# Optimization experiments

Hardware: AMD Instinct MI355X
Metric: run time of the kernel (lower is better)

The kernel has to match this reference:

```python
import jax, jax.numpy as jnp
import numpy as np

N_NODES = 100000
N_EDGES = 1600000
D_FEAT = 128
HIDDEN = 64


def setup_inputs() -> dict:
    key = jax.random.key(0)
    k1, k2, k3, k4, k5 = jax.random.split(key, 5)
    x = jax.random.normal(k1, (N_NODES, D_FEAT), dtype=jnp.float32)
    edge_index = jax.random.randint(k2, (2, N_EDGES), 0, N_NODES, dtype=jnp.int32)
    edge_weight = jax.random.uniform(k3, (N_EDGES,), dtype=jnp.float32)
    W1 = jax.random.normal(k4, (D_FEAT, HIDDEN), dtype=jnp.float32) / np.sqrt(D_FEAT)
    b1 = jnp.zeros((HIDDEN,), dtype=jnp.float32)
    W2 = jax.random.normal(k5, (HIDDEN, 1), dtype=jnp.float32) / np.sqrt(HIDDEN)
    b2 = jnp.zeros((1,), dtype=jnp.float32)
    return {"x": x, "edge_index": edge_index, "edge_weight": edge_weight,
            "W1": W1, "b1": b1, "W2": W2, "b2": b2}


def reference(x, edge_index, edge_weight, W1, b1, W2, b2):
    N = x.shape[0]
    # PyG GCNConv default: add self-loops with weight 1.0
    loops = jnp.arange(N, dtype=edge_index.dtype)
    row = jnp.concatenate([edge_index[0], loops])  # source nodes
    col = jnp.concatenate([edge_index[1], loops])  # target nodes
    ew = jnp.concatenate([edge_weight, jnp.ones((N,), dtype=edge_weight.dtype)])
    # symmetric degree normalization: norm_e = d^{-1/2}[row] * w_e * d^{-1/2}[col]
    deg = jax.ops.segment_sum(ew, col, num_segments=N)
    dinv = jnp.where(deg > 0, jax.lax.rsqrt(deg), 0.0)
    norm = dinv[row] * ew * dinv[col]  # [E+N]

    def gcn_layer(h, W, b):
        h = h @ W                          # [N, out] transform first (PyG order)
        msg = h[row] * norm[:, None]       # gather + scale, [E+N, out]
        agg = jax.ops.segment_sum(msg, col, num_segments=N)  # scatter-add
        return agg + b

    h = jax.nn.relu(gcn_layer(x, W1, b1))
    # dropout(p=0.5) is identity in eval mode
    return gcn_layer(h, W2, b2)  # [N, 1]
```

## Files before the change

kernel.cpp:

```cpp
#include <hip/hip_runtime.h>
#include <stdint.h>

typedef float f4 __attribute__((ext_vector_type(4)));
typedef float f32x4 __attribute__((ext_vector_type(4)));
typedef _Float16 hq4 __attribute__((ext_vector_type(4)));
typedef _Float16 half8 __attribute__((ext_vector_type(8)));

#define DF 128
#define HID 64
#define EPB 4096
#define CAP 5120

__global__ __launch_bounds__(256) void kPrep(const float* __restrict__ W1,
                                             _Float16* __restrict__ W1f,
                                             int* __restrict__ cur, int nbin) {
    int t = blockIdx.x * 256 + threadIdx.x;
    if (t < nbin) cur[t] = 0;
    if (t < 8192) {
        int j     = t & 7;
        int lane  = (t >> 3) & 63;
        int ntile = (t >> 9) & 3;
        int kstep = t >> 11;
        int k = kstep * 32 + (lane >> 4) * 8 + j;
        int n = ntile * 16 + (lane & 15);
        W1f[t] = (_Float16)W1[k * 64 + n];
    }
}

__global__ __launch_bounds__(512) void kA3(const int* __restrict__ row,
                                           const int* __restrict__ col,
                                           const float* __restrict__ ew,
                                           int* __restrict__ cur,
                                           int2* __restrict__ tmp,
                                           int E, int nbin) {
    __shared__ int hist[512];
    __shared__ int pref[512];
    __shared__ int lbase[512];
    __shared__ int2 sv[EPB];
    __shared__ int  sa[EPB];
    int b = blockIdx.x, t = threadIdx.x;
    hist[t] = 0;
    __syncthreads();
    int s = b * EPB, e = min(E, s + EPB);
    int cnt = e - s;
    int  mybin[8], myrank[8];
    int2 myv[8];
#pragma unroll
    for (int k = 0; k < 8; ++k) {
        int i = s + t + k * 512;
        mybin[k] = -1;
        if (i < e) {
            int c = col[i];
            int bin = c >> 8;
            myv[k].x = row[i] | ((c & 255) << 24);
            myv[k].y = __float_as_int(ew[i]);
            mybin[k] = bin;
            myrank[k] = atomicAdd(&hist[bin], 1);
        }
    }
    __syncthreads();
    int val = hist[t];
    lbase[t] = val ? atomicAdd(&cur[t], val) + t * CAP : 0;
    for (int d = 1; d < 512; d <<= 1) {
        int x = (t >= d) ? hist[t - d] : 0;
        __syncthreads();
        hist[t] += x;
        __syncthreads();
    }
    pref[t] = hist[t] - val;
    __syncthreads();
#pragma unroll
    for (int k = 0; k < 8; ++k) {
        if (mybin[k] >= 0) {
            int pos = pref[mybin[k]] + myrank[k];
            sv[pos] = myv[k];
            sa[pos] = lbase[mybin[k]] + myrank[k];
        }
    }
    __syncthreads();
    for (int i = t; i < cnt; i += 512) tmp[sa[i]] = sv[i];
}

__global__ __launch_bounds__(256) void kB(const int2* __restrict__ tmp,
                                          const int* __restrict__ cur,
                                          int2* __restrict__ edata,
                                          int2* __restrict__ offse,
                                          float* __restrict__ dinv,
                                          int N) {
    __shared__ int hist[256];
    __shared__ int basel[256];
    __shared__ int startl[256];
    __shared__ float degl[256];
    __shared__ int2 sorted[CAP];
    int bin = blockIdx.x, t = threadIdx.x;
    int s = bin * CAP;
    int cnt = min(cur[bin], CAP);
    int e = s + cnt;

    hist[t] = 0;
    degl[t] = 0.f;
    __syncthreads();
    for (int i = s + t; i < e; i += 256) {
        int2 pr = tmp[i];
        int lo = ((unsigned)pr.x) >> 24;
        atomicAdd(&hist[lo], 1);
        atomicAdd(&degl[lo], __int_as_float(pr.y));
    }
    __syncthreads();
    int val = hist[t];
    __syncthreads();
    for (int d = 1; d < 256; d <<= 1) {
        int x = (t >= d) ? hist[t - d] : 0;
        __syncthreads();
        hist[t] += x;
        __syncthreads();
    }
    int loff = hist[t] - val;
    startl[t] = s + loff;
    basel[t]  = loff;
    __syncthreads();
    for (int i = s + t; i < e; i += 256) {
        int2 pr = tmp[i];
        int lo = ((unsigned)pr.x) >> 24;
        int pos = atomicAdd(&basel[lo], 1);
        int2 o;
        o.x = pr.x & 0x00FFFFFF;
        o.y = pr.y;
        sorted[pos] = o;
    }
    __syncthreads();
    for (int i = t; i < cnt; i += 256) edata[s + i] = sorted[i];
    int c = bin * 256 + t;
    if (c < N) {
        int2 oe;
        oe.x = startl[t];
        oe.y = startl[t] + val;
        offse[c] = oe;
        dinv[c] = rsqrtf(1.0f + degl[t]);
    }
}

__global__ __launch_bounds__(256) void k_gemm1(const float* __restrict__ x,
                                               const _Float16* __restrict__ W1f,
                                               const float* __restrict__ dinv,
                                               _Float16* __restrict__ h, int N) {
    int wave  = (blockIdx.x * 256 + threadIdx.x) >> 6;
    int nstrip = (N + 15) >> 4;
    if (wave >= nstrip) return;
    int node0 = wave << 4;
    int l = threadIdx.x & 63;
    int quad = l >> 4;
    int m = l & 15;
    int r = node0 + m;
    if (r >= N) r = N - 1;

    const half8* bfrag = (const half8*)W1f;
    f32x4 acc[4];
#pragma unroll
    for (int nt = 0; nt < 4; ++nt) acc[nt] = (f32x4)(0.f);

#pragma unroll
    for (int kstep = 0; kstep < 4; ++kstep) {
        const f4* xr = (const f4*)(x + (size_t)r * DF + kstep * 32 + quad * 8);
        f4 a0 = xr[0], a1 = xr[1];
        half8 af;
        af[0] = (_Float16)a0.x; af[1] = (_Float16)a0.y;
        af[2] = (_Float16)a0.z; af[3] = (_Float16)a0.w;
        af[4] = (_Float16)a1.x; af[5] = (_Float16)a1.y;
        af[6] = (_Float16)a1.z; af[7] = (_Float16)a1.w;
#pragma unroll
        for (int nt = 0; nt < 4; ++nt) {
            half8 bf = bfrag[(kstep * 4 + nt) * 64 + l];
            acc[nt] = __builtin_amdgcn_mfma_f32_16x16x32_f16(af, bf, acc[nt], 0, 0, 0);
        }
    }

    float dv[4];
    int nodeb = node0 + quad * 4;
#pragma unroll
    for (int reg = 0; reg < 4; ++reg)
        dv[reg] = (nodeb + reg < N) ? dinv[nodeb + reg] : 0.f;
#pragma unroll
    for (int nt = 0; nt < 4; ++nt) {
#pragma unroll
        for (int reg = 0; reg < 4; ++reg) {
            int node = nodeb + reg;
            if (node < N)
                h[(unsigned)node * 64u + (unsigned)(nt * 16 + m)] =
                    (_Float16)(dv[reg] * acc[nt][reg]);
        }
    }
}

__global__ __launch_bounds__(256) void k_agg_h2(const int2* __restrict__ offse,
                                                const int2* __restrict__ edata,
                                                const float* __restrict__ dinv,
                                                const _Float16* __restrict__ h,
                                                const float* __restrict__ b1,
                                                const float* __restrict__ W2,
                                                float* __restrict__ h2p, int N) {
    __shared__ int2 stage[4][64];
    int wv = threadIdx.x >> 6;
    int v = blockIdx.x * 4 + wv;
    if (v >= N) return;
    int l = threadIdx.x & 63;
    int sub = l >> 4;
    unsigned fq = (unsigned)(l & 15);
    const hq4* hp = (const hq4*)h;

    float di = dinv[v];
    float a0 = 0.f, a1 = 0.f, a2 = 0.f, a3 = 0.f;
    if (sub == 0) {
        hq4 sv4 = hp[((unsigned)v << 4) | fq];
        a0 = (float)sv4.x; a1 = (float)sv4.y;
        a2 = (float)sv4.z; a3 = (float)sv4.w;
    }

    int2 oe = offse[v];
    for (int base = oe.x; base < oe.y; base += 64) {
        int idx = base + l;
        int2 pr;
        pr.x = 0; pr.y = 0;
        if (idx < oe.y) pr = edata[idx];
        stage[wv][l] = pr;
        int cnt = min(64, oe.y - base);
        int steps = (cnt + 3) >> 2;
#pragma unroll 4
        for (int k = 0; k < steps; ++k) {
            int2 em = stage[wv][4 * k + sub];
            float w = __int_as_float(em.y);
            hq4 hv = hp[((unsigned)em.x << 4) | fq];
            a0 += w * (float)hv.x;
            a1 += w * (float)hv.y;
            a2 += w * (float)hv.z;
            a3 += w * (float)hv.w;
        }
    }
    a0 += __shfl_xor(a0, 16); a1 += __shfl_xor(a1, 16);
    a2 += __shfl_xor(a2, 16); a3 += __shfl_xor(a3, 16);
    a0 += __shfl_xor(a0, 32); a1 += __shfl_xor(a1, 32);
    a2 += __shfl_xor(a2, 32); a3 += __shfl_xor(a3, 32);

    if (sub == 0) {
        a0 = di * a0; a1 = di * a1; a2 = di * a2; a3 = di * a3;
        float s = fmaxf(a0 + b1[4 * fq], 0.f)     * W2[4 * fq]
                + fmaxf(a1 + b1[4 * fq + 1], 0.f) * W2[4 * fq + 1]
                + fmaxf(a2 + b1[4 * fq + 2], 0.f) * W2[4 * fq + 2]
                + fmaxf(a3 + b1[4 * fq + 3], 0.f) * W2[4 * fq + 3];
        s += __shfl_down(s, 8);
        s += __shfl_down(s, 4);
        s += __shfl_down(s, 2);
        s += __shfl_down(s, 1);
        if (fq == 0) h2p[v] = di * s;
    }
}

__global__ __launch_bounds__(256) void k_out(const int2* __restrict__ offse,
                                             const int2* __restrict__ edata,
                                             const float* __restrict__ dinv,
                                             const float* __restrict__ h2p,
                                             const float* __restrict__ b2,
                                             float* __restrict__ out, int N) {
    int t = blockIdx.x * 256 + threadIdx.x;
    int v = t >> 4;
    if (v >= N) return;
    int c = t & 15;
    int2 oe = offse[v];
    float s = 0.f;
    for (int i = oe.x + c; i < oe.y; i += 16) {
        int2 pr = edata[i];
        s += __int_as_float(pr.y) * h2p[(unsigned)pr.x];
    }
    s += __shfl_down(s, 8);
    s += __shfl_down(s, 4);
    s += __shfl_down(s, 2);
    s += __shfl_down(s, 1);
    if (c == 0) {
        float di = dinv[v];
        out[v] = b2[0] + di * (h2p[v] + s);
    }
}

extern "C" void kernel_launch(void* const* d_in, const int* in_sizes, int n_in,
                              void* d_out, int out_size, void* d_ws, size_t ws_size,
                              hipStream_t stream) {
    const float* x  = (const float*)d_in[0];
    const int*   ei = (const int*)d_in[1];
    const float* ew = (const float*)d_in[2];
    const float* W1 = (const float*)d_in[3];
    const float* b1 = (const float*)d_in[4];
    const float* W2 = (const float*)d_in[5];
    const float* b2 = (const float*)d_in[6];
    float* out = (float*)d_out;

    const int N = in_sizes[0] / DF;
    const int E = in_sizes[2];
    const int* row = ei;
    const int* col = ei + E;

    const int nbin = (N + 255) / 256;
    const int nblk = (E + EPB - 1) / EPB;

    size_t    gsz   = (size_t)nbin * CAP;
    int*      w32   = (int*)d_ws;
    int2*     edata = (int2*)w32;
    int*      shreg = w32 + (size_t)2 * gsz;
    int2*     tmp   = (int2*)shreg;
    _Float16* h     = (_Float16*)shreg;
    int*      p     = shreg + (size_t)2 * gsz;
    int*      cur   = p;  p += ((nbin) + 3) & ~3;
    float*    dinv  = (float*)p;  p += N;
    float*    h2p   = (float*)p;  p += N;
    int2*     offse = (int2*)p;   p += 2 * N;
    _Float16* W1f   = (_Float16*)p;

    const int B = 256;
    int nstrip = (N + 15) / 16;
    int gGm  = (nstrip + 3) / 4;
    int gAgg = (N + 3) / 4;
    int gN16 = (N * 16 + B - 1) / B;

    kPrep<<<32, B, 0, stream>>>(W1, W1f, cur, nbin);
    kA3<<<nblk, 512, 0, stream>>>(row, col, ew, cur, tmp, E, nbin);
    kB<<<nbin, B, 0, stream>>>(tmp, cur, edata, offse, dinv, N);
    k_gemm1<<<gGm, B, 0, stream>>>(x, W1f, dinv, h, N);
    k_agg_h2<<<gAgg, B, 0, stream>>>(offse, edata, dinv, h, b1, W2, h2p, N);
    k_out<<<gN16, B, 0, stream>>>(offse, edata, dinv, h2p, b2, out, N);
}
```

Measured before the change: 207.5 us.

## Assign one 16-lane group per node in hidden-layer aggregation kernel

Remaps k_agg_h2 so each 16-lane group handles one destination node, with four nodes per wave, instead of one wave per node split into four edge subgroups. Edges are staged in padded LDS per group and processed with a fully unrolled 16-edge loop, removing the cross-subgroup shuffle reduction and the idle lanes in the epilogue. b1/W2 are read as float4. The trade-off is padding waste for degrees that are not multiples of 16 and divergence between groups with different degrees in the same wave.

```diff
diff --git a/kernel.cpp b/kernel.cpp
--- a/kernel.cpp
+++ b/kernel.cpp
@@ -199,35 +199,34 @@
                                                 const float* __restrict__ b1,
                                                 const float* __restrict__ W2,
                                                 float* __restrict__ h2p, int N) {
-    __shared__ int2 stage[4][64];
+    __shared__ int2 stage[4][68];
     int wv = threadIdx.x >> 6;
-    int v = blockIdx.x * 4 + wv;
-    if (v >= N) return;
-    int l = threadIdx.x & 63;
-    int sub = l >> 4;
+    int l  = threadIdx.x & 63;
+    int g  = l >> 4;
     unsigned fq = (unsigned)(l & 15);
+    int sbase = g * 17;
+    int vv = blockIdx.x * 16 + wv * 4 + g;
+    bool ok = vv < N;
+    int v = ok ? vv : N - 1;
     const hq4* hp = (const hq4*)h;
 
     float di = dinv[v];
-    float a0 = 0.f, a1 = 0.f, a2 = 0.f, a3 = 0.f;
-    if (sub == 0) {
-        hq4 sv4 = hp[((unsigned)v << 4) | fq];
-        a0 = (float)sv4.x; a1 = (float)sv4.y;
-        a2 = (float)sv4.z; a3 = (float)sv4.w;
-    }
-
     int2 oe = offse[v];
-    for (int base = oe.x; base < oe.y; base += 64) {
-        int idx = base + l;
+
+    hq4 sv4 = hp[((unsigned)v << 4) | fq];
+    float a0 = (float)sv4.x, a1 = (float)sv4.y;
+    float a2 = (float)sv4.z, a3 = (float)sv4.w;
+
+    int deg = oe.y - oe.x;
+    for (int base = 0; base < deg; base += 16) {
+        int idx = oe.x + base + (int)fq;
         int2 pr;
         pr.x = 0; pr.y = 0;
         if (idx < oe.y) pr = edata[idx];
-        stage[wv][l] = pr;
-        int cnt = min(64, oe.y - base);
-        int steps = (cnt + 3) >> 2;
-#pragma unroll 4
-        for (int k = 0; k < steps; ++k) {
-            int2 em = stage[wv][4 * k + sub];
+        stage[wv][sbase + (int)fq] = pr;
+#pragma unroll
+        for (int k = 0; k < 16; ++k) {
+            int2 em = stage[wv][sbase + k];
             float w = __int_as_float(em.y);
             hq4 hv = hp[((unsigned)em.x << 4) | fq];
             a0 += w * (float)hv.x;
@@ -236,23 +235,19 @@
             a3 += w * (float)hv.w;
         }
     }
-    a0 += __shfl_xor(a0, 16); a1 += __shfl_xor(a1, 16);
-    a2 += __shfl_xor(a2, 16); a3 += __shfl_xor(a3, 16);
-    a0 += __shfl_xor(a0, 32); a1 += __shfl_xor(a1, 32);
-    a2 += __shfl_xor(a2, 32); a3 += __shfl_xor(a3, 32);
-
-    if (sub == 0) {
-        a0 = di * a0; a1 = di * a1; a2 = di * a2; a3 = di * a3;
-        float s = fmaxf(a0 + b1[4 * fq], 0.f)     * W2[4 * fq]
-                + fmaxf(a1 + b1[4 * fq + 1], 0.f) * W2[4 * fq + 1]
-                + fmaxf(a2 + b1[4 * fq + 2], 0.f) * W2[4 * fq + 2]
-                + fmaxf(a3 + b1[4 * fq + 3], 0.f) * W2[4 * fq + 3];
-        s += __shfl_down(s, 8);
-        s += __shfl_down(s, 4);
-        s += __shfl_down(s, 2);
-        s += __shfl_down(s, 1);
-        if (fq == 0) h2p[v] = di * s;
-    }
+
+    a0 = di * a0; a1 = di * a1; a2 = di * a2; a3 = di * a3;
+    f4 bb = ((const f4*)b1)[fq];
+    f4 ww = ((const f4*)W2)[fq];
+    float s = fmaxf(a0 + bb.x, 0.f) * ww.x
+            + fmaxf(a1 + bb.y, 0.f) * ww.y
+            + fmaxf(a2 + bb.z, 0.f) * ww.z
+            + fmaxf(a3 + bb.w, 0.f) * ww.w;
+    s += __shfl_down(s, 8);
+    s += __shfl_down(s, 4);
+    s += __shfl_down(s, 2);
+    s += __shfl_down(s, 1);
+    if (fq == 0 && ok) h2p[vv] = di * s;
 }
 
 __global__ __launch_bounds__(256) void k_out(const int2* __restrict__ offse,
@@ -317,7 +312,7 @@
     const int B = 256;
     int nstrip = (N + 15) / 16;
     int gGm  = (nstrip + 3) / 4;
-    int gAgg = (N + 3) / 4;
+    int gAgg = (N + 15) / 16;
     int gN16 = (N * 16 + B - 1) / B;
 
     kPrep<<<32, B, 0, stream>>>(W1, W1f, cur, nbin);
```

New measurement: 193.2 us. 6.9% less time.
